# Kernel optimization log

Hardware: AMD Instinct MI355X
Metric: run time of the kernel (lower is better)

Reference implementation:

```python
import jax, jax.numpy as jnp
import numpy as np

B, S, DIM = 64, 256, 512
H = 16
DH = DIM // H          # 32
W = 256                # window_size == seq_len
ROPE_BASE = 10000.0


def _rope(x):
    # x: (B, S, H, DH), interleaved-pair RoPE
    pos = jnp.arange(S, dtype=jnp.float32)
    inv_freq = 1.0 / (ROPE_BASE ** (jnp.arange(0, DH, 2, dtype=jnp.float32) / DH))
    sinusoid = pos[:, None] * inv_freq[None, :]            # (S, DH/2)
    sin = jnp.sin(sinusoid)[None, :, None, :]              # (1, S, 1, DH/2)
    cos = jnp.cos(sinusoid)[None, :, None, :]
    x1 = x[..., 0::2]
    x2 = x[..., 1::2]
    r1 = x1 * cos - x2 * sin
    r2 = x1 * sin + x2 * cos
    return jnp.stack([r1, r2], axis=-1).reshape(x.shape)


def setup_inputs() -> dict:
    key = jax.random.key(0)
    ks = jax.random.split(key, 8)
    s = 1.0 / np.sqrt(DIM)
    return {
        "hidden_states": jax.random.normal(ks[0], (B, S, DIM), jnp.float32),
        "Wq": jax.random.normal(ks[1], (DIM, DIM), jnp.float32) * s,
        "bq": jnp.zeros((DIM,), jnp.float32),
        "Wk": jax.random.normal(ks[2], (DIM, DIM), jnp.float32) * s,
        "bk": jnp.zeros((DIM,), jnp.float32),
        "Wv": jax.random.normal(ks[3], (DIM, DIM), jnp.float32) * s,
        "bv": jnp.zeros((DIM,), jnp.float32),
        "bias_table": jax.random.normal(ks[4], (2 * W - 1, H), jnp.float32) * 0.02,
    }


def reference(hidden_states, Wq, bq, Wk, bk, Wv, bv, bias_table):
    b, s, _ = hidden_states.shape
    q = hidden_states @ Wq + bq
    k = hidden_states @ Wk + bk
    v = hidden_states @ Wv + bv
    # (B, S, H, DH)
    q = _rope(q.reshape(b, s, H, DH))
    k = _rope(k.reshape(b, s, H, DH))
    v = v.reshape(b, s, H, DH)
    # (B, H, S, DH)
    q = q.transpose(0, 2, 1, 3)
    k = k.transpose(0, 2, 1, 3)
    v = v.transpose(0, 2, 1, 3)
    scores = jnp.einsum('bhqd,bhkd->bhqk', q, k) / np.sqrt(DH)
    # relative_position_index[i, j] == (i - j) + W - 1
    rel_idx = jnp.arange(W)[:, None] - jnp.arange(W)[None, :] + (W - 1)
    rel_bias = bias_table[rel_idx]                 # (W, W, H)
    rel_bias = rel_bias.transpose(2, 0, 1)[None]   # (1, H, W, W)
    # NOTE: bias added AFTER softmax, faithful to the original module
    probs = jax.nn.softmax(scores, axis=-1) + rel_bias
    ctx = jnp.einsum('bhqk,bhkd->bhqd', probs, v)
    ctx = ctx.transpose(0, 2, 1, 3).reshape(b, s, DIM)
    return ctx
```

## Files before the change

kernel.cpp:

```cpp
#include <hip/hip_runtime.h>
#include <stdint.h>

typedef __attribute__((ext_vector_type(8))) short bf16x8;
typedef __attribute__((ext_vector_type(4))) float f32x4;
typedef __attribute__((ext_vector_type(4))) unsigned int u32x4;

#define MFMA16(a, b, c) __builtin_amdgcn_mfma_f32_16x16x32_bf16(a, b, c, 0, 0, 0)

__device__ __forceinline__ float bf2f(unsigned short u) {
    union { unsigned int i; float f; } x; x.i = ((unsigned int)u) << 16; return x.f;
}
__device__ __forceinline__ unsigned short f2bf(float f) {
    union { float f; unsigned int i; } x; x.f = f;
    unsigned int u = x.i;
    return (unsigned short)((u + 0x7FFFu + ((u >> 16) & 1u)) >> 16);
}

__global__ __launch_bounds__(256) void k_cvt(const float4* __restrict__ in,
                                             unsigned short* __restrict__ out) {
    int i = blockIdx.x * 256 + threadIdx.x;
    float4 v = in[i];
    ushort4 o;
    o.x = f2bf(v.x); o.y = f2bf(v.y); o.z = f2bf(v.z); o.w = f2bf(v.w);
    *(ushort4*)(out + (size_t)i * 4) = o;
}

__global__ __launch_bounds__(256) void k_wt(const float* __restrict__ W0,
                                            const float* __restrict__ W1,
                                            const float* __restrict__ W2,
                                            unsigned short* __restrict__ Wt) {
    __shared__ float t[64][65];
    const float* Wm = (blockIdx.z == 0) ? W0 : (blockIdx.z == 1) ? W1 : W2;
    int k0 = blockIdx.x * 64, n0 = blockIdx.y * 64;
    for (int it = 0; it < 16; ++it) {
        int idx = threadIdx.x + it * 256;
        int r = idx >> 6, c = idx & 63;
        t[r][c] = Wm[(k0 + r) * 512 + n0 + c];
    }
    __syncthreads();
    unsigned short* dst = Wt + (size_t)blockIdx.z * 512 * 512;
    for (int it = 0; it < 16; ++it) {
        int idx = threadIdx.x + it * 256;
        int nr = idx >> 6, kc = idx & 63;
        dst[(n0 + nr) * 512 + k0 + kc] = f2bf(t[kc][nr]);
    }
}

__global__ __launch_bounds__(256) void k_sc(float* __restrict__ cs2) {
    int s = threadIdx.x;
    for (int f = 0; f < 16; ++f) {
        float inv = powf(10000.0f, -(float)f / 16.0f);
        float a = (float)s * inv;
        cs2[(s * 16 + f) * 2 + 0] = cosf(a);
        cs2[(s * 16 + f) * 2 + 1] = sinf(a);
    }
}

__global__ __launch_bounds__(256, 2) void k_gemm(
    const unsigned short* __restrict__ A,
    const unsigned short* __restrict__ Bw,
    const float* __restrict__ bq, const float* __restrict__ bk, const float* __restrict__ bv,
    const float* __restrict__ cs2,
    unsigned short* __restrict__ Qo, unsigned short* __restrict__ Ko, unsigned short* __restrict__ Vo) {
    __shared__ unsigned short a_l[2][8192];
    __shared__ unsigned short b_l[2][8192];
    const int tid = threadIdx.x;
    const int wave = tid >> 6, lane = tid & 63;
    const int l15 = lane & 15, l4 = lane >> 4;
    int bid = blockIdx.x;
    int swz = (bid & 7) * 192 + (bid >> 3);
    const int m0 = (swz / 12) * 128;
    const int n0 = (swz % 12) * 128;
    const int wm = (wave >> 1) * 64, wn = (wave & 1) * 64;
    const bool isV = (n0 >= 1024);

    f32x4 zero4 = {0.f, 0.f, 0.f, 0.f};
    f32x4 acc[4][4];
#pragma unroll
    for (int i = 0; i < 4; ++i)
#pragma unroll
        for (int j = 0; j < 4; ++j) acc[i][j] = zero4;

    const int srow = tid >> 3;
    const int skc = ((tid & 7) ^ (srow & 7)) * 8;
    const unsigned short* ga = A + (size_t)(m0 + srow) * 512 + skc;
    const unsigned short* gb = Bw + (size_t)(n0 + srow) * 512 + skc;

#define STAGE(buf, kt)                                                                          \
    {                                                                                           \
        const unsigned short* pa = ga + (kt) * 64;                                              \
        const unsigned short* pb = gb + (kt) * 64;                                              \
        unsigned short* la = &a_l[(buf)][wave * 512];                                           \
        unsigned short* lb = &b_l[(buf)][wave * 512];                                           \
        _Pragma("unroll")                                                                       \
        for (int it = 0; it < 4; ++it) {                                                        \
            __builtin_amdgcn_global_load_lds(                                                   \
                (const __attribute__((address_space(1))) unsigned int*)(pa + it * (32 * 512)),  \
                (__attribute__((address_space(3))) unsigned int*)(la + it * 2048), 16, 0, 0);   \
            __builtin_amdgcn_global_load_lds(                                                   \
                (const __attribute__((address_space(1))) unsigned int*)(pb + it * (32 * 512)),  \
                (__attribute__((address_space(3))) unsigned int*)(lb + it * 2048), 16, 0, 0);   \
        }                                                                                       \
    }

    STAGE(0, 0);
    __syncthreads();
    int cur = 0;
    for (int kt = 0; kt < 8; ++kt) {
        if (kt < 7) STAGE(cur ^ 1, kt + 1);
#pragma unroll
        for (int kc = 0; kc < 2; ++kc) {
            bf16x8 af[4], bfr[4];
#pragma unroll
            for (int i = 0; i < 4; ++i) {
                int g = ((kc * 4 + l4) ^ (l15 & 7)) * 8;
                af[i] = *(const bf16x8*)&a_l[cur][(wm + i * 16 + l15) * 64 + g];
            }
#pragma unroll
            for (int j = 0; j < 4; ++j) {
                int g = ((kc * 4 + l4) ^ (l15 & 7)) * 8;
                bfr[j] = *(const bf16x8*)&b_l[cur][(wn + j * 16 + l15) * 64 + g];
            }
            if (!isV) {
#pragma unroll
                for (int i = 0; i < 4; ++i)
#pragma unroll
                    for (int j = 0; j < 4; ++j) acc[i][j] = MFMA16(af[i], bfr[j], acc[i][j]);
            } else {
#pragma unroll
                for (int i = 0; i < 4; ++i)
#pragma unroll
                    for (int j = 0; j < 4; ++j) acc[i][j] = MFMA16(bfr[j], af[i], acc[i][j]);
            }
        }
        __syncthreads();
        cur ^= 1;
    }
#undef STAGE

    if (!isV) {
        const int mat = n0 >> 9;
        unsigned short* __restrict__ dst = (mat == 0) ? Qo : Ko;
        const float* __restrict__ bias = (mat == 0) ? bq : bk;
#pragma unroll
        for (int j = 0; j < 4; ++j) {
            int col = (n0 & 511) + wn + j * 16 + l15;
            float bb = bias[col];
            int h = col >> 5, dh = col & 31, f = dh >> 1;
            float sgn = (col & 1) ? 1.0f : -1.0f;
#pragma unroll
            for (int i = 0; i < 4; ++i) {
#pragma unroll
                for (int r = 0; r < 4; ++r) {
                    int m = m0 + wm + i * 16 + l4 * 4 + r;
                    int b = m >> 8, s = m & 255;
                    float t = acc[i][j][r] + bb;
                    float partner = __shfl_xor(t, 1);
                    float2 cn = *(const float2*)(cs2 + (s * 16 + f) * 2);
                    float o = t * cn.x + sgn * partner * cn.y;
                    dst[(size_t)(b * 16 + h) * 8192 + s * 32 + dh] = f2bf(o);
                }
            }
        }
    } else {
#pragma unroll
        for (int j = 0; j < 4; ++j) {
#pragma unroll
            for (int r = 0; r < 4; ++r) {
                int n = (n0 & 511) + wn + j * 16 + l4 * 4 + r;
                float bb = bv[n];
                int h = n >> 5, dh = n & 31;
#pragma unroll
                for (int i = 0; i < 4; ++i) {
                    int m = m0 + wm + i * 16 + l15;
                    int b = m >> 8, s = m & 255;
                    Vo[(size_t)(b * 16 + h) * 8192 + dh * 256 + s] = f2bf(acc[i][j][r] + bb);
                }
            }
        }
    }
}

__global__ __launch_bounds__(256, 2) void k_attn(
    const unsigned short* __restrict__ Qm, const unsigned short* __restrict__ Km,
    const unsigned short* __restrict__ Vm,
    const float* __restrict__ bias_table, float* __restrict__ out) {
    __shared__ unsigned short k_l[256 * 32];
    __shared__ unsigned short vt_l[32 * 256];
    __shared__ unsigned short p_l[64 * 264];
    __shared__ float bias_l[320];

    const int tid = threadIdx.x, wave = tid >> 6, lane = tid & 63;
    const int l15 = lane & 15, l4 = lane >> 4;
    int bid = blockIdx.x;
    int swz = (bid & 7) * 512 + (bid >> 3);
    const int qb = swz & 3, h = (swz >> 2) & 15, b = swz >> 6;
    const int q0 = qb * 64;
    const size_t bh = ((size_t)(b * 16 + h)) * 8192;

    for (int i = tid; i < 319; i += 256) bias_l[i] = bias_table[(q0 + i) * 16 + h];

#pragma unroll
    for (int it = 0; it < 4; ++it) {
        int p = it * 256 + wave * 64 + lane;
        __builtin_amdgcn_global_load_lds(
            (const __attribute__((address_space(1))) unsigned int*)(Km + bh + p * 8),
            (__attribute__((address_space(3))) unsigned int*)(k_l + it * 2048 + wave * 512), 16, 0, 0);
    }
#pragma unroll
    for (int it = 0; it < 4; ++it) {
        int p = it * 256 + wave * 64 + lane;
        int dh = p >> 5, cpos = p & 31;
        int srcc = cpos ^ (dh & 7);
        __builtin_amdgcn_global_load_lds(
            (const __attribute__((address_space(1))) unsigned int*)(Vm + bh + dh * 256 + srcc * 8),
            (__attribute__((address_space(3))) unsigned int*)(vt_l + it * 2048 + wave * 512), 16, 0, 0);
    }

    bf16x8 qfrag = *(const bf16x8*)(Qm + bh + (size_t)(q0 + 16 * wave + l15) * 32 + l4 * 8);
    __syncthreads();

    f32x4 zero4 = {0.f, 0.f, 0.f, 0.f};
    f32x4 sc[16];
#pragma unroll
    for (int ct = 0; ct < 16; ++ct) {
        bf16x8 kf = *(const bf16x8*)&k_l[(ct * 16 + l15) * 32 + l4 * 8];
        sc[ct] = MFMA16(kf, qfrag, zero4);
    }

    const float SCL2 = 0.17677669529663687f * 1.4426950408889634f;
    float sum = 0.f;
#pragma unroll
    for (int ct = 0; ct < 16; ++ct) {
#pragma unroll
        for (int r = 0; r < 4; ++r) {
            float e;
            float x = sc[ct][r] * SCL2;
            asm("v_exp_f32 %0, %1" : "=v"(e) : "v"(x));
            sc[ct][r] = e;
            sum += e;
        }
    }
    sum += __shfl_xor(sum, 16);
    sum += __shfl_xor(sum, 32);
    float inv = 1.0f / sum;

    const int qrow = 16 * wave + l15;
#pragma unroll
    for (int ct = 0; ct < 16; ++ct) {
        int kbase = 16 * ct + 4 * l4;
        int jb = qrow - kbase + 255;
        float p0 = sc[ct][0] * inv + bias_l[jb];
        float p1 = sc[ct][1] * inv + bias_l[jb - 1];
        float p2 = sc[ct][2] * inv + bias_l[jb - 2];
        float p3 = sc[ct][3] * inv + bias_l[jb - 3];
        uint2 w;
        w.x = (unsigned int)f2bf(p0) | ((unsigned int)f2bf(p1) << 16);
        w.y = (unsigned int)f2bf(p2) | ((unsigned int)f2bf(p3) << 16);
        *(uint2*)&p_l[qrow * 264 + kbase] = w;
    }

    f32x4 o0 = zero4, o1 = zero4;
#pragma unroll
    for (int kc = 0; kc < 8; ++kc) {
        bf16x8 pf = *(const bf16x8*)&p_l[qrow * 264 + kc * 32 + l4 * 8];
        int vc = (kc * 4 + l4) ^ (l15 & 7);
        bf16x8 v0 = *(const bf16x8*)&vt_l[l15 * 256 + vc * 8];
        bf16x8 v1 = *(const bf16x8*)&vt_l[(16 + l15) * 256 + vc * 8];
        o0 = MFMA16(pf, v0, o0);
        o1 = MFMA16(pf, v1, o1);
    }

#pragma unroll
    for (int r = 0; r < 4; ++r) {
        int s = q0 + 16 * wave + l4 * 4 + r;
        float* po = out + ((size_t)(b * 256 + s)) * 512 + h * 32;
        po[l15] = o0[r];
        po[16 + l15] = o1[r];
    }
}

extern "C" void kernel_launch(void* const* d_in, const int* in_sizes, int n_in,
                              void* d_out, int out_size, void* d_ws, size_t ws_size,
                              hipStream_t stream) {
    const float* hs = (const float*)d_in[0];
    const float* Wq = (const float*)d_in[1];
    const float* bq = (const float*)d_in[2];
    const float* Wk = (const float*)d_in[3];
    const float* bk = (const float*)d_in[4];
    const float* Wv = (const float*)d_in[5];
    const float* bv = (const float*)d_in[6];
    const float* bt = (const float*)d_in[7];
    float* out = (float*)d_out;

    char* ws = (char*)d_ws;
    unsigned short* hsb = (unsigned short*)ws;
    unsigned short* wt = (unsigned short*)(ws + 16777216);
    unsigned short* Qo = (unsigned short*)(ws + 18350080);
    unsigned short* Ko = (unsigned short*)(ws + 35127296);
    unsigned short* Vo = (unsigned short*)(ws + 51904512);
    float* cs2 = (float*)(ws + 68681728);

    hipLaunchKernelGGL(k_cvt, dim3(8192), dim3(256), 0, stream, (const float4*)hs, hsb);
    hipLaunchKernelGGL(k_wt, dim3(8, 8, 3), dim3(256), 0, stream, Wq, Wk, Wv, wt);
    hipLaunchKernelGGL(k_sc, dim3(1), dim3(256), 0, stream, cs2);
    hipLaunchKernelGGL(k_gemm, dim3(1536), dim3(256), 0, stream,
                       hsb, wt, bq, bk, bv, cs2, Qo, Ko, Vo);
    hipLaunchKernelGGL(k_attn, dim3(4096), dim3(256), 0, stream,
                       Qo, Ko, Vo, bt, out);
}
```

Measured before the change: 98.38 us.

## Load GEMM B operand directly into registers, halve LDS, raise occupancy

The weight (B) tile is no longer staged through shared memory. Each lane loads its MFMA B fragments straight from global memory into double-buffered registers. This halves LDS use per block, and the launch bound rises to 3 blocks per CU, aiming for more occupancy and fewer LDS reads. The cost is more VGPR pressure, uncoalesced 16-byte global loads that repeat across waves, and explicit waitcnt barriers that block until all loads drain.

Measured after the change: 225.2 us. 129% more time.

```diff
diff --git a/kernel.cpp b/kernel.cpp
--- a/kernel.cpp
+++ b/kernel.cpp
@@ -56,14 +56,13 @@
     }
 }
 
-__global__ __launch_bounds__(256, 2) void k_gemm(
+__global__ __launch_bounds__(256, 3) void k_gemm(
     const unsigned short* __restrict__ A,
     const unsigned short* __restrict__ Bw,
     const float* __restrict__ bq, const float* __restrict__ bk, const float* __restrict__ bv,
     const float* __restrict__ cs2,
     unsigned short* __restrict__ Qo, unsigned short* __restrict__ Ko, unsigned short* __restrict__ Vo) {
     __shared__ unsigned short a_l[2][8192];
-    __shared__ unsigned short b_l[2][8192];
     const int tid = threadIdx.x;
     const int wave = tid >> 6, lane = tid & 63;
     const int l15 = lane & 15, l4 = lane >> 4;
@@ -84,59 +83,73 @@
     const int srow = tid >> 3;
     const int skc = ((tid & 7) ^ (srow & 7)) * 8;
     const unsigned short* ga = A + (size_t)(m0 + srow) * 512 + skc;
-    const unsigned short* gb = Bw + (size_t)(n0 + srow) * 512 + skc;
+    const unsigned short* gB = Bw + (size_t)(n0 + wn + l15) * 512 + l4 * 8;
 
 #define STAGE(buf, kt)                                                                          \
     {                                                                                           \
         const unsigned short* pa = ga + (kt) * 64;                                              \
-        const unsigned short* pb = gb + (kt) * 64;                                              \
         unsigned short* la = &a_l[(buf)][wave * 512];                                           \
-        unsigned short* lb = &b_l[(buf)][wave * 512];                                           \
         _Pragma("unroll")                                                                       \
         for (int it = 0; it < 4; ++it) {                                                        \
             __builtin_amdgcn_global_load_lds(                                                   \
                 (const __attribute__((address_space(1))) unsigned int*)(pa + it * (32 * 512)),  \
                 (__attribute__((address_space(3))) unsigned int*)(la + it * 2048), 16, 0, 0);   \
-            __builtin_amdgcn_global_load_lds(                                                   \
-                (const __attribute__((address_space(1))) unsigned int*)(pb + it * (32 * 512)),  \
-                (__attribute__((address_space(3))) unsigned int*)(lb + it * 2048), 16, 0, 0);   \
         }                                                                                       \
     }
-
+#define LOADB(breg, kt)                                                                         \
+    {                                                                                           \
+        _Pragma("unroll")                                                                       \
+        for (int kc = 0; kc < 2; ++kc)                                                          \
+            _Pragma("unroll")                                                                   \
+            for (int j = 0; j < 4; ++j)                                                         \
+                breg[kc][j] = *(const bf16x8*)(gB + (size_t)j * 8192 + (kt) * 64 + kc * 32);    \
+    }
+#define COMPUTE(buf, breg)                                                                      \
+    {                                                                                           \
+        _Pragma("unroll")                                                                       \
+        for (int kc = 0; kc < 2; ++kc) {                                                        \
+            bf16x8 af[4];                                                                       \
+            int g = ((kc * 4 + l4) ^ (l15 & 7)) * 8;                                            \
+            _Pragma("unroll")                                                                   \
+            for (int i = 0; i < 4; ++i)                                                         \
+                af[i] = *(const bf16x8*)&a_l[(buf)][(wm + i * 16 + l15) * 64 + g];              \
+            if (!isV) {                                                                         \
+                _Pragma("unroll")                                                               \
+                for (int i = 0; i < 4; ++i)                                                     \
+                    _Pragma("unroll")                                                           \
+                    for (int j = 0; j < 4; ++j)                                                 \
+                        acc[i][j] = MFMA16(af[i], breg[kc][j], acc[i][j]);                      \
+            } else {                                                                            \
+                _Pragma("unroll")                                                               \
+                for (int i = 0; i < 4; ++i)                                                     \
+                    _Pragma("unroll")                                                           \
+                    for (int j = 0; j < 4; ++j)                                                 \
+                        acc[i][j] = MFMA16(breg[kc][j], af[i], acc[i][j]);                      \
+            }                                                                                   \
+        }                                                                                       \
+    }
+#define SYNC() { asm volatile("s_waitcnt vmcnt(0) lgkmcnt(0)" ::: "memory");                    \
+                 __builtin_amdgcn_s_barrier(); }
+
+    bf16x8 b0[2][4], b1[2][4];
+    LOADB(b0, 0);
     STAGE(0, 0);
-    __syncthreads();
-    int cur = 0;
-    for (int kt = 0; kt < 8; ++kt) {
-        if (kt < 7) STAGE(cur ^ 1, kt + 1);
-#pragma unroll
-        for (int kc = 0; kc < 2; ++kc) {
-            bf16x8 af[4], bfr[4];
-#pragma unroll
-            for (int i = 0; i < 4; ++i) {
-                int g = ((kc * 4 + l4) ^ (l15 & 7)) * 8;
-                af[i] = *(const bf16x8*)&a_l[cur][(wm + i * 16 + l15) * 64 + g];
-            }
-#pragma unroll
-            for (int j = 0; j < 4; ++j) {
-                int g = ((kc * 4 + l4) ^ (l15 & 7)) * 8;
-                bfr[j] = *(const bf16x8*)&b_l[cur][(wn + j * 16 + l15) * 64 + g];
-            }
-            if (!isV) {
-#pragma unroll
-                for (int i = 0; i < 4; ++i)
-#pragma unroll
-                    for (int j = 0; j < 4; ++j) acc[i][j] = MFMA16(af[i], bfr[j], acc[i][j]);
-            } else {
-#pragma unroll
-                for (int i = 0; i < 4; ++i)
-#pragma unroll
-                    for (int j = 0; j < 4; ++j) acc[i][j] = MFMA16(bfr[j], af[i], acc[i][j]);
-            }
+    for (int kt2 = 0; kt2 < 8; kt2 += 2) {
+        SYNC();
+        LOADB(b1, kt2 + 1);
+        STAGE(1, kt2 + 1);
+        COMPUTE(0, b0);
+        SYNC();
+        if (kt2 + 2 < 8) {
+            LOADB(b0, kt2 + 2);
+            STAGE(0, kt2 + 2);
         }
-        __syncthreads();
-        cur ^= 1;
+        COMPUTE(1, b1);
     }
 #undef STAGE
+#undef LOADB
+#undef COMPUTE
+#undef SYNC
 
     if (!isV) {
         const int mat = n0 >> 9;
```

## Loop attention over all query blocks per head and keep probabilities in registers

Applied to the files above, without the earlier changes.

The attention kernel now launches one block per (batch, head) and loops over the four 64-row query blocks. K, V and the bias column are loaded into LDS once and reused, where before each block reloaded them. The probability tile no longer goes through LDS: lane shuffles rearrange the packed bf16 values into the MFMA A-operand layout, and the conversion uses v_cvt_pk_bf16_f32. Launch bounds rise to 3 blocks per CU, but the grid shrinks to 1024 blocks and each block's query blocks run serially, which cuts parallelism.

New measurement: 96.47 us. Within noise of the previous version (-1.9%).

```diff
diff --git a/kernel.cpp b/kernel.cpp
--- a/kernel.cpp
+++ b/kernel.cpp
@@ -153,12 +153,12 @@
 #pragma unroll
                 for (int r = 0; r < 4; ++r) {
                     int m = m0 + wm + i * 16 + l4 * 4 + r;
-                    int b = m >> 8, s = m & 255;
+                    int b2 = m >> 8, s = m & 255;
                     float t = acc[i][j][r] + bb;
                     float partner = __shfl_xor(t, 1);
                     float2 cn = *(const float2*)(cs2 + (s * 16 + f) * 2);
                     float o = t * cn.x + sgn * partner * cn.y;
-                    dst[(size_t)(b * 16 + h) * 8192 + s * 32 + dh] = f2bf(o);
+                    dst[(size_t)(b2 * 16 + h) * 8192 + s * 32 + dh] = f2bf(o);
                 }
             }
         }
@@ -173,32 +173,30 @@
 #pragma unroll
                 for (int i = 0; i < 4; ++i) {
                     int m = m0 + wm + i * 16 + l15;
-                    int b = m >> 8, s = m & 255;
-                    Vo[(size_t)(b * 16 + h) * 8192 + dh * 256 + s] = f2bf(acc[i][j][r] + bb);
+                    int b2 = m >> 8, s = m & 255;
+                    Vo[(size_t)(b2 * 16 + h) * 8192 + dh * 256 + s] = f2bf(acc[i][j][r] + bb);
                 }
             }
         }
     }
 }
 
-__global__ __launch_bounds__(256, 2) void k_attn(
+__global__ __launch_bounds__(256, 3) void k_attn(
     const unsigned short* __restrict__ Qm, const unsigned short* __restrict__ Km,
     const unsigned short* __restrict__ Vm,
     const float* __restrict__ bias_table, float* __restrict__ out) {
     __shared__ unsigned short k_l[256 * 32];
     __shared__ unsigned short vt_l[32 * 256];
-    __shared__ unsigned short p_l[64 * 264];
-    __shared__ float bias_l[320];
+    __shared__ float bias_g[512];
 
     const int tid = threadIdx.x, wave = tid >> 6, lane = tid & 63;
     const int l15 = lane & 15, l4 = lane >> 4;
     int bid = blockIdx.x;
-    int swz = (bid & 7) * 512 + (bid >> 3);
-    const int qb = swz & 3, h = (swz >> 2) & 15, b = swz >> 6;
-    const int q0 = qb * 64;
+    int swz = (bid & 7) * 128 + (bid >> 3);
+    const int h = swz & 15, b = swz >> 4;
     const size_t bh = ((size_t)(b * 16 + h)) * 8192;
 
-    for (int i = tid; i < 319; i += 256) bias_l[i] = bias_table[(q0 + i) * 16 + h];
+    for (int i = tid; i < 511; i += 256) bias_g[i] = bias_table[i * 16 + h];
 
 #pragma unroll
     for (int it = 0; it < 4; ++it) {
@@ -216,67 +214,87 @@
             (const __attribute__((address_space(1))) unsigned int*)(Vm + bh + dh * 256 + srcc * 8),
             (__attribute__((address_space(3))) unsigned int*)(vt_l + it * 2048 + wave * 512), 16, 0, 0);
     }
-
-    bf16x8 qfrag = *(const bf16x8*)(Qm + bh + (size_t)(q0 + 16 * wave + l15) * 32 + l4 * 8);
     __syncthreads();
 
     f32x4 zero4 = {0.f, 0.f, 0.f, 0.f};
-    f32x4 sc[16];
-#pragma unroll
-    for (int ct = 0; ct < 16; ++ct) {
-        bf16x8 kf = *(const bf16x8*)&k_l[(ct * 16 + l15) * 32 + l4 * 8];
-        sc[ct] = MFMA16(kf, qfrag, zero4);
-    }
-
     const float SCL2 = 0.17677669529663687f * 1.4426950408889634f;
-    float sum = 0.f;
-#pragma unroll
-    for (int ct = 0; ct < 16; ++ct) {
+    const int qrow = 16 * wave + l15;
+    const bool hi = (l4 >> 1) != 0;
+    const bool odd = (l4 & 1) != 0;
+
+    for (int qb = 0; qb < 4; ++qb) {
+        const int q0 = qb * 64;
+        bf16x8 qfrag = *(const bf16x8*)(Qm + bh + (size_t)(q0 + qrow) * 32 + l4 * 8);
+
+        f32x4 sc[16];
+#pragma unroll
+        for (int ct = 0; ct < 16; ++ct) {
+            bf16x8 kf = *(const bf16x8*)&k_l[(ct * 16 + l15) * 32 + l4 * 8];
+            sc[ct] = MFMA16(kf, qfrag, zero4);
+        }
+
+        float sum = 0.f;
+#pragma unroll
+        for (int ct = 0; ct < 16; ++ct) {
+#pragma unroll
+            for (int r = 0; r < 4; ++r) {
+                float e;
+                float x = sc[ct][r] * SCL2;
+                asm("v_exp_f32 %0, %1" : "=v"(e) : "v"(x));
+                sc[ct][r] = e;
+                sum += e;
+            }
+        }
+        sum += __shfl_xor(sum, 16);
+        sum += __shfl_xor(sum, 32);
+        float inv = 1.0f / sum;
+
+        f32x4 o0 = zero4, o1 = zero4;
+#pragma unroll
+        for (int m = 0; m < 8; ++m) {
+            unsigned int E0, E1, O0, O1;
+            {
+                int kbase = 32 * m + 4 * l4;
+                int jb = q0 + qrow - kbase + 255;
+                float p0 = sc[2 * m][0] * inv + bias_g[jb];
+                float p1 = sc[2 * m][1] * inv + bias_g[jb - 1];
+                float p2 = sc[2 * m][2] * inv + bias_g[jb - 2];
+                float p3 = sc[2 * m][3] * inv + bias_g[jb - 3];
+                asm("v_cvt_pk_bf16_f32 %0, %1, %2" : "=v"(E0) : "v"(p0), "v"(p1));
+                asm("v_cvt_pk_bf16_f32 %0, %1, %2" : "=v"(E1) : "v"(p2), "v"(p3));
+                jb -= 16;
+                p0 = sc[2 * m + 1][0] * inv + bias_g[jb];
+                p1 = sc[2 * m + 1][1] * inv + bias_g[jb - 1];
+                p2 = sc[2 * m + 1][2] * inv + bias_g[jb - 2];
+                p3 = sc[2 * m + 1][3] * inv + bias_g[jb - 3];
+                asm("v_cvt_pk_bf16_f32 %0, %1, %2" : "=v"(O0) : "v"(p0), "v"(p1));
+                asm("v_cvt_pk_bf16_f32 %0, %1, %2" : "=v"(O1) : "v"(p2), "v"(p3));
+            }
+            unsigned int m0_ = hi ? O0 : E0, m1_ = hi ? O1 : E1;
+            unsigned int s0 = hi ? E0 : O0, s1 = hi ? E1 : O1;
+            unsigned int g0 = __shfl_xor(s0, 32), g1 = __shfl_xor(s1, 32);
+            unsigned int X00 = hi ? g0 : m0_, X01 = hi ? g1 : m1_;
+            unsigned int X10 = hi ? m0_ : g0, X11 = hi ? m1_ : g1;
+            unsigned int k0 = odd ? X10 : X00, k1 = odd ? X11 : X01;
+            unsigned int t0 = odd ? X00 : X10, t1 = odd ? X01 : X11;
+            unsigned int r0 = __shfl_xor(t0, 16), r1 = __shfl_xor(t1, 16);
+            union { unsigned int u[4]; bf16x8 v; } pu;
+            pu.u[0] = odd ? r0 : k0; pu.u[1] = odd ? r1 : k1;
+            pu.u[2] = odd ? k0 : r0; pu.u[3] = odd ? k1 : r1;
+            int vc = (m * 4 + l4) ^ (l15 & 7);
+            bf16x8 v0 = *(const bf16x8*)&vt_l[l15 * 256 + vc * 8];
+            bf16x8 v1 = *(const bf16x8*)&vt_l[(16 + l15) * 256 + vc * 8];
+            o0 = MFMA16(pu.v, v0, o0);
+            o1 = MFMA16(pu.v, v1, o1);
+        }
+
 #pragma unroll
         for (int r = 0; r < 4; ++r) {
-            float e;
-            float x = sc[ct][r] * SCL2;
-            asm("v_exp_f32 %0, %1" : "=v"(e) : "v"(x));
-            sc[ct][r] = e;
-            sum += e;
-        }
-    }
-    sum += __shfl_xor(sum, 16);
-    sum += __shfl_xor(sum, 32);
-    float inv = 1.0f / sum;
-
-    const int qrow = 16 * wave + l15;
-#pragma unroll
-    for (int ct = 0; ct < 16; ++ct) {
-        int kbase = 16 * ct + 4 * l4;
-        int jb = qrow - kbase + 255;
-        float p0 = sc[ct][0] * inv + bias_l[jb];
-        float p1 = sc[ct][1] * inv + bias_l[jb - 1];
-        float p2 = sc[ct][2] * inv + bias_l[jb - 2];
-        float p3 = sc[ct][3] * inv + bias_l[jb - 3];
-        uint2 w;
-        w.x = (unsigned int)f2bf(p0) | ((unsigned int)f2bf(p1) << 16);
-        w.y = (unsigned int)f2bf(p2) | ((unsigned int)f2bf(p3) << 16);
-        *(uint2*)&p_l[qrow * 264 + kbase] = w;
-    }
-
-    f32x4 o0 = zero4, o1 = zero4;
-#pragma unroll
-    for (int kc = 0; kc < 8; ++kc) {
-        bf16x8 pf = *(const bf16x8*)&p_l[qrow * 264 + kc * 32 + l4 * 8];
-        int vc = (kc * 4 + l4) ^ (l15 & 7);
-        bf16x8 v0 = *(const bf16x8*)&vt_l[l15 * 256 + vc * 8];
-        bf16x8 v1 = *(const bf16x8*)&vt_l[(16 + l15) * 256 + vc * 8];
-        o0 = MFMA16(pf, v0, o0);
-        o1 = MFMA16(pf, v1, o1);
-    }
-
-#pragma unroll
-    for (int r = 0; r < 4; ++r) {
-        int s = q0 + 16 * wave + l4 * 4 + r;
-        float* po = out + ((size_t)(b * 256 + s)) * 512 + h * 32;
-        po[l15] = o0[r];
-        po[16 + l15] = o1[r];
+            int s = q0 + 16 * wave + l4 * 4 + r;
+            float* po = out + ((size_t)(b * 256 + s)) * 512 + h * 32;
+            po[l15] = o0[r];
+            po[16 + l15] = o1[r];
+        }
     }
 }
 
@@ -306,6 +324,6 @@
     hipLaunchKernelGGL(k_sc, dim3(1), dim3(256), 0, stream, cs2);
     hipLaunchKernelGGL(k_gemm, dim3(1536), dim3(256), 0, stream,
                        hsb, wt, bq, bk, bv, cs2, Qo, Ko, Vo);
-    hipLaunchKernelGGL(k_attn, dim3(4096), dim3(256), 0, stream,
+    hipLaunchKernelGGL(k_attn, dim3(1024), dim3(256), 0, stream,
                        Qo, Ko, Vo, bt, out);
 }
```
